# Kernel tuning notes

Measured on AMD Instinct MI355X. Metric: run time of the kernel, lower is better.

## Reference

```python
import jax, jax.numpy as jnp
import numpy as np

L, H, P, R = 8192, 1024, 512, 256


def setup_inputs() -> dict:
    key = jax.random.key(0)
    ks = jax.random.split(key, 12)
    nrm = lambda k, s, std=0.01: std * jax.random.normal(k, s, dtype=jnp.float32)
    # Stable complex diagonal: |Lambda_bar| in [0.8, 0.999)
    mag = 0.8 + 0.199 * jax.random.uniform(ks[8], (P,), dtype=jnp.float32)
    phase = jnp.pi * jax.random.uniform(ks[9], (P,), dtype=jnp.float32)
    return {
        "input_sequence": jax.random.normal(ks[0], (L, H), dtype=jnp.float32),
        "F": nrm(ks[1], (R, H)),
        "H_proj": nrm(ks[2], (R, H)),
        "Delta_p": jnp.eye(R, dtype=jnp.float32),
        "Delta_r": jnp.eye(R, dtype=jnp.float32),
        "E": nrm(ks[3], (P, R)),
        "G": nrm(ks[4], (H, R)),
        "Lambda_bar_re": (mag * jnp.cos(phase)).astype(jnp.float32),
        "Lambda_bar_im": (mag * jnp.sin(phase)).astype(jnp.float32),
        "B_bar_re": nrm(ks[5], (P, H), 0.05),
        "B_bar_im": nrm(ks[6], (P, H), 0.05),
        "C_re": nrm(ks[7], (H, P), 0.05),
        "C_im": nrm(ks[10], (H, P), 0.05),
        "D": nrm(ks[11], (H, H), 0.02),
    }


def _binop(a, b):
    # Diagonal linear SSM associative combine: (lam, bu)
    return (b[0] * a[0], b[0] * a[1] + b[1])


def reference(input_sequence, F, H_proj, Delta_p, Delta_r, E, G,
              Lambda_bar_re, Lambda_bar_im, B_bar_re, B_bar_im,
              C_re, C_im, D):
    # p_k = Delta_p @ (F @ u_k), r_k = Delta_r @ (H_proj @ u_k)  -- vmapped over L via matmul
    p_seq = (input_sequence @ F.T) @ Delta_p.T            # (L, R)
    r_seq = (input_sequence @ H_proj.T) @ Delta_r.T       # (L, R)
    up_seq = jnp.concatenate([input_sequence, p_seq], axis=-1)  # (L, H+R)

    Lam = (Lambda_bar_re + 1j * Lambda_bar_im).astype(jnp.complex64)         # (P,)
    B_bar = (B_bar_re + 1j * B_bar_im).astype(jnp.complex64)                 # (P, H)
    B_ext = jnp.concatenate([B_bar, E.astype(jnp.complex64)], axis=1)        # (P, H+R)

    # Per-step driving term Bu_k = B_ext @ up_k
    Bu = up_seq.astype(jnp.complex64) @ B_ext.T                               # (L, P)
    Lam_el = jnp.broadcast_to(Lam, Bu.shape)                                  # (L, P)

    # Parallel associative scan: x_k = Lam * x_{k-1} + Bu_k
    _, xs = jax.lax.associative_scan(_binop, (Lam_el, Bu))                    # (L, P)

    C_tilde = (C_re + 1j * C_im).astype(jnp.complex64)                        # (H, P)
    # conj_sym=True branch: y_k = 2*Re(C_tilde @ x_k) + G @ r_k + D @ u_k
    y_seq = (2.0 * jnp.real(xs @ C_tilde.T)
             + r_seq @ G.T
             + input_sequence @ D.T)                                           # (L, H)
    return y_seq
```

## Files before the change

### kernel.cpp

```cpp
#include <hip/hip_runtime.h>
#include <stdint.h>

#define L_SEQ 8192
#define NCHUNK 64
#define CHUNK  128

typedef __attribute__((ext_vector_type(8))) short bf16x8;
typedef __attribute__((ext_vector_type(4))) float f32x4;

__device__ inline unsigned short f2bf(float x) {
  unsigned u = __builtin_bit_cast(unsigned, x);
  unsigned r = (u + 0x7fffu + ((u >> 16) & 1u)) >> 16;
  return (unsigned short)r;
}
__device__ inline float bf2f(unsigned short b) {
  unsigned u = ((unsigned)b) << 16;
  return __builtin_bit_cast(float, u);
}

#define GLD16(g, l)                                                            \
  __builtin_amdgcn_global_load_lds(                                            \
      (const __attribute__((address_space(1))) unsigned int*)(g),              \
      (__attribute__((address_space(3))) unsigned int*)(l), 16, 0, 0)

__global__ __launch_bounds__(256) void prep(
    const float* __restrict__ F, const float* __restrict__ Hp,
    const float* __restrict__ dP, const float* __restrict__ dR,
    const float* __restrict__ E, const float* __restrict__ G,
    const float* __restrict__ Bim, const float* __restrict__ Cre,
    const float* __restrict__ Cim, const float* __restrict__ u,
    unsigned short* __restrict__ Ft, unsigned short* __restrict__ Ht,
    unsigned short* __restrict__ dPb, unsigned short* __restrict__ dRb,
    unsigned short* __restrict__ Eb, unsigned short* __restrict__ Gb,
    unsigned short* __restrict__ W1, unsigned short* __restrict__ Wy,
    unsigned short* __restrict__ A2) {
  __shared__ float tile[32][33];
  const int b = blockIdx.x, tid = threadIdx.x;
  if (b < 512) {
    const float* src = (b < 256) ? F : Hp;
    unsigned short* dst = (b < 256) ? Ft : Ht;
    int bb = b & 255;
    int bx = bb & 31, by = bb >> 5;
    int tx = tid & 31, ty = tid >> 5;
#pragma unroll
    for (int dy = 0; dy < 32; dy += 8)
      tile[ty + dy][tx] = src[(size_t)(by * 32 + ty + dy) * 1024 + bx * 32 + tx];
    __syncthreads();
#pragma unroll
    for (int dy = 0; dy < 32; dy += 8)
      dst[(size_t)(bx * 32 + ty + dy) * 256 + by * 32 + tx] = f2bf(tile[tx][ty + dy]);
    return;
  }
  if (b < 1024) {
    const float* src;
    unsigned short* dst;
    int q;
    if (b < 576)      { src = dP; dst = dPb; q = (b - 512) * 256 + tid; }
    else if (b < 640) { src = dR; dst = dRb; q = (b - 576) * 256 + tid; }
    else if (b < 768) { src = E;  dst = Eb;  q = (b - 640) * 256 + tid; }
    else              { src = G;  dst = Gb;  q = (b - 768) * 256 + tid; }
    int e = q * 4;
    float4 v = *(const float4*)(src + e);
    ushort4 o = {f2bf(v.x), f2bf(v.y), f2bf(v.z), f2bf(v.w)};
    *(ushort4*)(dst + e) = o;
    return;
  }
  if (b < 1536) {
    int q = (b - 1024) * 256 + tid;
    int e = q * 4, p = e >> 10, j = e & 1023;
    float4 v = *(const float4*)(Bim + (size_t)p * 1024 + j);
    ushort4 o = {f2bf(v.x), f2bf(v.y), f2bf(v.z), f2bf(v.w)};
    *(ushort4*)(W1 + (size_t)(2 * p + 1) * 1024 + j) = o;
    return;
  }
  if (b < 2560) {
    int q = (b - 1536) * 256 + tid;
    int i = q >> 8, jp = (q & 255) * 2;
    float2 re = *(const float2*)(Cre + (size_t)i * 512 + jp);
    float2 im = *(const float2*)(Cim + (size_t)i * 512 + jp);
    ushort4 o = {f2bf(2.f * re.x), f2bf(-2.f * im.x), f2bf(2.f * re.y), f2bf(-2.f * im.y)};
    *(ushort4*)(Wy + (size_t)i * 2048 + 1024 + 2 * jp) = o;
    return;
  }
  {
    int q = (b - 2560) * 256 + tid;
    int e = q * 4, i = e >> 10, j = e & 1023;
    float4 v = *(const float4*)(u + (size_t)i * 1024 + j);
    ushort4 o = {f2bf(v.x), f2bf(v.y), f2bf(v.z), f2bf(v.w)};
    *(ushort4*)(A2 + (size_t)i * 2048 + j) = o;
  }
}

template <int HAS_ADD, int OUT_F32, int OUT_BF16>
__device__ __forceinline__ void gemm_body(
    const unsigned short* __restrict__ A, int lda,
    const unsigned short* __restrict__ B, int ldb,
    float* __restrict__ C, int ldc,
    unsigned short* __restrict__ Cb, int ldcb,
    const float* __restrict__ Add, int ldadd, int K, int m0, int n0,
    unsigned short* sA, unsigned short* sB) {
  const int tid = threadIdx.x;
  const int lane = tid & 63, wave = tid >> 6;
  const int wm = wave >> 1, wn = wave & 1;
  const int frow = lane & 15, fg = lane >> 4;

  const int srow = lane >> 2;
  const int scol = (lane & 3) * 8;
  const unsigned short* gA0 = A + (size_t)(m0 + wave * 32 + srow) * lda + scol;
  const unsigned short* gA1 = gA0 + (size_t)16 * lda;
  const unsigned short* gB0 = B + (size_t)(n0 + wave * 32 + srow) * ldb + scol;
  const unsigned short* gB1 = gB0 + (size_t)16 * ldb;

  f32x4 acc[4][4] = {};
  const int nt = K >> 5;

  {
    unsigned short* a0 = sA + wave * 1024;
    unsigned short* b0 = sB + wave * 1024;
    GLD16(gA0, a0); GLD16(gA1, a0 + 512);
    GLD16(gB0, b0); GLD16(gB1, b0 + 512);
  }
  __syncthreads();

  for (int t = 0; t < nt; ++t) {
    const int cur = (t & 1) * 4096;
    if (t + 1 < nt) {
      const int nxt = 4096 - cur;
      const int kt = (t + 1) * 32;
      unsigned short* a0 = sA + nxt + wave * 1024;
      unsigned short* b0 = sB + nxt + wave * 1024;
      GLD16(gA0 + kt, a0); GLD16(gA1 + kt, a0 + 512);
      GLD16(gB0 + kt, b0); GLD16(gB1 + kt, b0 + 512);
    }
    const unsigned short* bA = sA + cur;
    const unsigned short* bB = sB + cur;
    bf16x8 fa[4], fb[4];
#pragma unroll
    for (int f = 0; f < 4; ++f) {
      fa[f] = *(const bf16x8*)(bA + (wm * 64 + f * 16 + frow) * 32 + fg * 8);
      fb[f] = *(const bf16x8*)(bB + (wn * 64 + f * 16 + frow) * 32 + fg * 8);
    }
#pragma unroll
    for (int i = 0; i < 4; ++i)
#pragma unroll
      for (int j = 0; j < 4; ++j)
        acc[i][j] = __builtin_amdgcn_mfma_f32_16x16x32_bf16(fa[i], fb[j], acc[i][j], 0, 0, 0);
    __syncthreads();
  }

  const int crow4 = (lane >> 4) * 4, ccol = lane & 15;
#pragma unroll
  for (int i = 0; i < 4; ++i)
#pragma unroll
    for (int j = 0; j < 4; ++j)
#pragma unroll
      for (int q = 0; q < 4; ++q) {
        int r = m0 + wm * 64 + i * 16 + crow4 + q;
        int c = n0 + wn * 64 + j * 16 + ccol;
        float v = acc[i][j][q];
        if (HAS_ADD) v += Add[(size_t)r * ldadd + c];
        if (OUT_F32) C[(size_t)r * ldc + c] = v;
        if (OUT_BF16) Cb[(size_t)r * ldcb + c] = f2bf(v);
      }
}

template <int HAS_ADD, int OUT_F32, int OUT_BF16>
__global__ __launch_bounds__(256) void gemm_bt(
    const unsigned short* __restrict__ A, int lda,
    const unsigned short* __restrict__ B, int ldb,
    float* __restrict__ C, int ldc,
    unsigned short* __restrict__ Cb, int ldcb,
    const float* __restrict__ Add, int ldadd, int K) {
  __shared__ __align__(16) unsigned short sA[2 * 128 * 32];
  __shared__ __align__(16) unsigned short sB[2 * 128 * 32];
  gemm_body<HAS_ADD, OUT_F32, OUT_BF16>(A, lda, B, ldb, C, ldc, Cb, ldcb, Add,
                                        ldadd, K, blockIdx.x * 128,
                                        blockIdx.y * 128, sA, sB);
}

struct GemmP {
  const unsigned short* A; int lda;
  const unsigned short* B; int ldb;
  float* C; int ldc;
  unsigned short* Cb; int ldcb;
  const float* Add; int ldadd;
  int K; int gx;
};

template <int HAS_ADD, int OUT_F32, int OUT_BF16>
__global__ __launch_bounds__(256) void gemm_bt_dual(GemmP p0, GemmP p1) {
  __shared__ __align__(16) unsigned short sA[2 * 128 * 32];
  __shared__ __align__(16) unsigned short sB[2 * 128 * 32];
  GemmP p = blockIdx.z ? p1 : p0;
  if ((int)blockIdx.x >= p.gx) return;
  gemm_body<HAS_ADD, OUT_F32, OUT_BF16>(p.A, p.lda, p.B, p.ldb, p.C, p.ldc,
                                        p.Cb, p.ldcb, p.Add, p.ldadd, p.K,
                                        blockIdx.x * 128, blockIdx.y * 128, sA, sB);
}

__global__ __launch_bounds__(256) void scan_carry(const unsigned short* __restrict__ Bub,
                                                  const float* __restrict__ lre,
                                                  const float* __restrict__ lim,
                                                  float2* __restrict__ carry2) {
  int g = blockIdx.x * 256 + threadIdx.x;
  int p = g & 511, c = g >> 9;
  float ar = lre[p], ai = lim[p];
  float sr = 0.f, si = 0.f;
  const unsigned short* base = Bub + (size_t)c * CHUNK * 1024 + 2 * p;
#pragma unroll 8
  for (int i = 0; i < CHUNK; ++i) {
    unsigned w = *(const unsigned*)(base + (size_t)i * 1024);
    float br = bf2f((unsigned short)(w & 0xffff));
    float bi = bf2f((unsigned short)(w >> 16));
    float nr = ar * sr - ai * si + br;
    float ni = ar * si + ai * sr + bi;
    sr = nr; si = ni;
  }
  carry2[(size_t)p * NCHUNK + c] = make_float2(sr, si);
}

__global__ __launch_bounds__(512) void scan_prefix(const float2* __restrict__ carry2,
                                                   const float* __restrict__ lre,
                                                   const float* __restrict__ lim,
                                                   float2* __restrict__ prefix2) {
  int p = threadIdx.x;
  float ar = lre[p], ai = lim[p];
  float cr = ar, ci = ai;
#pragma unroll
  for (int s = 0; s < 7; ++s) {
    float t = cr * cr - ci * ci;
    ci = 2.f * cr * ci;
    cr = t;
  }
  float sr = 0.f, si = 0.f;
  const float2* cp = carry2 + (size_t)p * NCHUNK;
  float2* pp = prefix2 + (size_t)p * NCHUNK;
  for (int cb = 0; cb < NCHUNK; cb += 16) {
    float2 cv[16];
#pragma unroll
    for (int i = 0; i < 16; ++i) cv[i] = cp[cb + i];
#pragma unroll
    for (int i = 0; i < 16; ++i) {
      float nr = cr * sr - ci * si + cv[i].x;
      float ni = cr * si + ci * sr + cv[i].y;
      sr = nr; si = ni;
      pp[cb + i] = make_float2(sr, si);
    }
  }
}

__global__ __launch_bounds__(256) void scan_apply(const unsigned short* __restrict__ Bub,
                                                  const float* __restrict__ lre,
                                                  const float* __restrict__ lim,
                                                  const float2* __restrict__ prefix2,
                                                  unsigned short* __restrict__ A2) {
  int g = blockIdx.x * 256 + threadIdx.x;
  int p = g & 511, c = g >> 9;
  float ar = lre[p], ai = lim[p];
  float sr = 0.f, si = 0.f;
  if (c > 0) {
    float2 pr = prefix2[(size_t)p * NCHUNK + c - 1];
    sr = pr.x; si = pr.y;
  }
  const unsigned short* base = Bub + (size_t)c * CHUNK * 1024 + 2 * p;
  unsigned* ob = (unsigned*)(A2 + (size_t)c * CHUNK * 2048 + 1024 + 2 * p);
#pragma unroll 8
  for (int i = 0; i < CHUNK; ++i) {
    unsigned w = *(const unsigned*)(base + (size_t)i * 1024);
    float br = bf2f((unsigned short)(w & 0xffff));
    float bi = bf2f((unsigned short)(w >> 16));
    float nr = ar * sr - ai * si + br;
    float ni = ar * si + ai * sr + bi;
    sr = nr; si = ni;
    ob[(size_t)i * 1024] = (unsigned)f2bf(sr) | ((unsigned)f2bf(si) << 16);
  }
}

extern "C" void kernel_launch(void* const* d_in, const int* in_sizes, int n_in,
                              void* d_out, int out_size, void* d_ws, size_t ws_size,
                              hipStream_t stream) {
  const float* u   = (const float*)d_in[0];
  const float* F   = (const float*)d_in[1];
  const float* Hp  = (const float*)d_in[2];
  const float* dP  = (const float*)d_in[3];
  const float* dR  = (const float*)d_in[4];
  const float* E   = (const float*)d_in[5];
  const float* G   = (const float*)d_in[6];
  const float* lre = (const float*)d_in[7];
  const float* lim = (const float*)d_in[8];
  const float* Bre = (const float*)d_in[9];
  const float* Bim = (const float*)d_in[10];
  const float* Cre = (const float*)d_in[11];
  const float* Cim = (const float*)d_in[12];
  const float* Dm  = (const float*)d_in[13];
  float* y = (float*)d_out;

  uint8_t* ws = (uint8_t*)d_ws;
  size_t off = 0;
  auto alloc = [&](size_t bytes) {
    void* p = ws + off;
    off += (bytes + 255) & ~(size_t)255;
    return p;
  };
  unsigned short* A2  = (unsigned short*)alloc((size_t)L_SEQ * 2048 * 2);
  unsigned short* W1  = (unsigned short*)alloc((size_t)1024 * 1024 * 2);
  unsigned short* Wy  = (unsigned short*)alloc((size_t)1024 * 2048 * 2);
  unsigned short* Bub = (unsigned short*)alloc((size_t)L_SEQ * 1024 * 2);
  unsigned short* Ft  = (unsigned short*)alloc((size_t)1024 * 256 * 2);
  unsigned short* Ht  = (unsigned short*)alloc((size_t)1024 * 256 * 2);
  unsigned short* FpT = (unsigned short*)alloc((size_t)1024 * 256 * 2);
  unsigned short* HrT = (unsigned short*)alloc((size_t)1024 * 256 * 2);
  unsigned short* dPb = (unsigned short*)alloc((size_t)256 * 256 * 2);
  unsigned short* dRb = (unsigned short*)alloc((size_t)256 * 256 * 2);
  unsigned short* Eb  = (unsigned short*)alloc((size_t)512 * 256 * 2);
  unsigned short* Gb  = (unsigned short*)alloc((size_t)1024 * 256 * 2);
  float* carry  = (float*)alloc((size_t)512 * NCHUNK * 8);
  float* prefix = (float*)alloc((size_t)512 * NCHUNK * 8);
  (void)ws_size; (void)in_sizes; (void)n_in; (void)out_size;

  prep<<<10752, 256, 0, stream>>>(F, Hp, dP, dR, E, G, Bim, Cre, Cim, u,
                                  Ft, Ht, dPb, dRb, Eb, Gb, W1, Wy, A2);

  GemmP pa = {Ft, 256, dPb, 256, nullptr, 0, FpT, 256, nullptr, 0, 256, 8};
  GemmP pb = {Ht, 256, dRb, 256, nullptr, 0, HrT, 256, nullptr, 0, 256, 8};
  gemm_bt_dual<0, 0, 1><<<dim3(8, 2, 2), 256, 0, stream>>>(pa, pb);

  GemmP pc = {Eb, 256, FpT, 256, nullptr, 0, W1, 2048, Bre, 1024, 256, 4};
  GemmP pd = {Gb, 256, HrT, 256, nullptr, 0, Wy, 2048, Dm, 1024, 256, 8};
  gemm_bt_dual<1, 0, 1><<<dim3(8, 8, 2), 256, 0, stream>>>(pc, pd);

  gemm_bt<0, 0, 1><<<dim3(64, 8), 256, 0, stream>>>(A2, 2048, W1, 1024, nullptr, 0,
                                                    Bub, 1024, nullptr, 0, 1024);

  scan_carry<<<128, 256, 0, stream>>>(Bub, lre, lim, (float2*)carry);
  scan_prefix<<<1, 512, 0, stream>>>((const float2*)carry, lre, lim, (float2*)prefix);
  scan_apply<<<128, 256, 0, stream>>>(Bub, lre, lim, (const float2*)prefix, A2);

  gemm_bt<0, 1, 0><<<dim3(64, 8), 256, 0, stream>>>(A2, 2048, Wy, 2048, y, 1024,
                                                    nullptr, 0, nullptr, 0, 2048);
}
```

Baseline: 241.0 us.

## Triple-buffer GEMM loads, swizzle blocks per XCD, fold small matmuls and scan prefix

The GEMM main loop moves from a double-buffered loop with a full barrier every step to a three-stage LDS pipeline that waits on vmcnt, so global loads stay in flight while MFMAs run. gemm_bt now remaps block indices so neighbouring tiles land on the same XCD, aiming for better L2 reuse. The weight pre-products E@Delta_p and G@Delta_r are computed directly in the prep kernel with a naive fp32 loop, and the reassociation (G·Δr)·H_proj replaces G·(Δr·H_proj), which removes one dual GEMM launch. The single-block scan_prefix kernel is dropped; each scan_apply thread now serially combines the earlier chunk carries itself, which adds redundant work in exchange for one fewer launch.

```diff
diff --git a/kernel.cpp b/kernel.cpp
--- a/kernel.cpp
+++ b/kernel.cpp
@@ -30,8 +30,7 @@
     const float* __restrict__ Bim, const float* __restrict__ Cre,
     const float* __restrict__ Cim, const float* __restrict__ u,
     unsigned short* __restrict__ Ft, unsigned short* __restrict__ Ht,
-    unsigned short* __restrict__ dPb, unsigned short* __restrict__ dRb,
-    unsigned short* __restrict__ Eb, unsigned short* __restrict__ Gb,
+    unsigned short* __restrict__ T1b, unsigned short* __restrict__ T2b,
     unsigned short* __restrict__ W1, unsigned short* __restrict__ Wy,
     unsigned short* __restrict__ A2) {
   __shared__ float tile[32][33];
@@ -52,29 +51,33 @@
     return;
   }
   if (b < 1024) {
-    const float* src;
-    unsigned short* dst;
-    int q;
-    if (b < 576)      { src = dP; dst = dPb; q = (b - 512) * 256 + tid; }
-    else if (b < 640) { src = dR; dst = dRb; q = (b - 576) * 256 + tid; }
-    else if (b < 768) { src = E;  dst = Eb;  q = (b - 640) * 256 + tid; }
-    else              { src = G;  dst = Gb;  q = (b - 768) * 256 + tid; }
-    int e = q * 4;
-    float4 v = *(const float4*)(src + e);
-    ushort4 o = {f2bf(v.x), f2bf(v.y), f2bf(v.z), f2bf(v.w)};
-    *(ushort4*)(dst + e) = o;
-    return;
-  }
-  if (b < 1536) {
-    int q = (b - 1024) * 256 + tid;
+    int i = b - 512, j = tid;
+    const float* Er = E + (size_t)i * 256;
+    float acc = 0.f;
+#pragma unroll 8
+    for (int k = 0; k < 256; ++k) acc += Er[k] * dP[(size_t)k * 256 + j];
+    T1b[(size_t)i * 256 + j] = f2bf(acc);
+    return;
+  }
+  if (b < 2048) {
+    int i = b - 1024, j = tid;
+    const float* Gr = G + (size_t)i * 256;
+    float acc = 0.f;
+#pragma unroll 8
+    for (int k = 0; k < 256; ++k) acc += Gr[k] * dR[(size_t)k * 256 + j];
+    T2b[(size_t)i * 256 + j] = f2bf(acc);
+    return;
+  }
+  if (b < 2560) {
+    int q = (b - 2048) * 256 + tid;
     int e = q * 4, p = e >> 10, j = e & 1023;
     float4 v = *(const float4*)(Bim + (size_t)p * 1024 + j);
     ushort4 o = {f2bf(v.x), f2bf(v.y), f2bf(v.z), f2bf(v.w)};
     *(ushort4*)(W1 + (size_t)(2 * p + 1) * 1024 + j) = o;
     return;
   }
-  if (b < 2560) {
-    int q = (b - 1536) * 256 + tid;
+  if (b < 3584) {
+    int q = (b - 2560) * 256 + tid;
     int i = q >> 8, jp = (q & 255) * 2;
     float2 re = *(const float2*)(Cre + (size_t)i * 512 + jp);
     float2 im = *(const float2*)(Cim + (size_t)i * 512 + jp);
@@ -83,7 +86,7 @@
     return;
   }
   {
-    int q = (b - 2560) * 256 + tid;
+    int q = (b - 3584) * 256 + tid;
     int e = q * 4, i = e >> 10, j = e & 1023;
     float4 v = *(const float4*)(u + (size_t)i * 1024 + j);
     ushort4 o = {f2bf(v.x), f2bf(v.y), f2bf(v.z), f2bf(v.w)};
@@ -114,26 +117,16 @@
   f32x4 acc[4][4] = {};
   const int nt = K >> 5;
 
-  {
-    unsigned short* a0 = sA + wave * 1024;
-    unsigned short* b0 = sB + wave * 1024;
-    GLD16(gA0, a0); GLD16(gA1, a0 + 512);
-    GLD16(gB0, b0); GLD16(gB1, b0 + 512);
-  }
-  __syncthreads();
-
-  for (int t = 0; t < nt; ++t) {
-    const int cur = (t & 1) * 4096;
-    if (t + 1 < nt) {
-      const int nxt = 4096 - cur;
-      const int kt = (t + 1) * 32;
-      unsigned short* a0 = sA + nxt + wave * 1024;
-      unsigned short* b0 = sB + nxt + wave * 1024;
-      GLD16(gA0 + kt, a0); GLD16(gA1 + kt, a0 + 512);
-      GLD16(gB0 + kt, b0); GLD16(gB1 + kt, b0 + 512);
-    }
-    const unsigned short* bA = sA + cur;
-    const unsigned short* bB = sB + cur;
+  auto STAGE = [&](int t, int buf) {
+    const int kt = t * 32;
+    unsigned short* a0 = sA + buf * 4096 + wave * 1024;
+    unsigned short* b0 = sB + buf * 4096 + wave * 1024;
+    GLD16(gA0 + kt, a0); GLD16(gA1 + kt, a0 + 512);
+    GLD16(gB0 + kt, b0); GLD16(gB1 + kt, b0 + 512);
+  };
+  auto COMPUTE = [&](int buf) {
+    const unsigned short* bA = sA + buf * 4096;
+    const unsigned short* bB = sB + buf * 4096;
     bf16x8 fa[4], fb[4];
 #pragma unroll
     for (int f = 0; f < 4; ++f) {
@@ -145,8 +138,27 @@
 #pragma unroll
       for (int j = 0; j < 4; ++j)
         acc[i][j] = __builtin_amdgcn_mfma_f32_16x16x32_bf16(fa[i], fb[j], acc[i][j], 0, 0, 0);
-    __syncthreads();
-  }
+  };
+
+  STAGE(0, 0);
+  if (nt > 1) STAGE(1, 1);
+
+  int buf = 0;
+  for (int t = 0; t < nt - 1; ++t) {
+    asm volatile("s_waitcnt vmcnt(4)" ::: "memory");
+    __builtin_amdgcn_s_barrier();
+    __builtin_amdgcn_sched_barrier(0);
+    if (t + 2 < nt) {
+      int b2 = buf + 2; if (b2 >= 3) b2 -= 3;
+      STAGE(t + 2, b2);
+    }
+    COMPUTE(buf);
+    if (++buf == 3) buf = 0;
+  }
+  asm volatile("s_waitcnt vmcnt(0)" ::: "memory");
+  __builtin_amdgcn_s_barrier();
+  __builtin_amdgcn_sched_barrier(0);
+  COMPUTE(buf);
 
   const int crow4 = (lane >> 4) * 4, ccol = lane & 15;
 #pragma unroll
@@ -171,11 +183,14 @@
     float* __restrict__ C, int ldc,
     unsigned short* __restrict__ Cb, int ldcb,
     const float* __restrict__ Add, int ldadd, int K) {
-  __shared__ __align__(16) unsigned short sA[2 * 128 * 32];
-  __shared__ __align__(16) unsigned short sB[2 * 128 * 32];
+  __shared__ __align__(16) unsigned short sA[3 * 128 * 32];
+  __shared__ __align__(16) unsigned short sB[3 * 128 * 32];
+  int lin = blockIdx.y * gridDim.x + blockIdx.x;
+  int xcd = lin & 7, idx = lin >> 3;
+  int bx = xcd * 8 + (idx & 7);
+  int by = idx >> 3;
   gemm_body<HAS_ADD, OUT_F32, OUT_BF16>(A, lda, B, ldb, C, ldc, Cb, ldcb, Add,
-                                        ldadd, K, blockIdx.x * 128,
-                                        blockIdx.y * 128, sA, sB);
+                                        ldadd, K, bx * 128, by * 128, sA, sB);
 }
 
 struct GemmP {
@@ -189,8 +204,8 @@
 
 template <int HAS_ADD, int OUT_F32, int OUT_BF16>
 __global__ __launch_bounds__(256) void gemm_bt_dual(GemmP p0, GemmP p1) {
-  __shared__ __align__(16) unsigned short sA[2 * 128 * 32];
-  __shared__ __align__(16) unsigned short sB[2 * 128 * 32];
+  __shared__ __align__(16) unsigned short sA[3 * 128 * 32];
+  __shared__ __align__(16) unsigned short sB[3 * 128 * 32];
   GemmP p = blockIdx.z ? p1 : p0;
   if ((int)blockIdx.x >= p.gx) return;
   gemm_body<HAS_ADD, OUT_F32, OUT_BF16>(p.A, p.lda, p.B, p.ldb, p.C, p.ldc,
@@ -216,14 +231,16 @@
     float ni = ar * si + ai * sr + bi;
     sr = nr; si = ni;
   }
-  carry2[(size_t)p * NCHUNK + c] = make_float2(sr, si);
-}
-
-__global__ __launch_bounds__(512) void scan_prefix(const float2* __restrict__ carry2,
-                                                   const float* __restrict__ lre,
-                                                   const float* __restrict__ lim,
-                                                   float2* __restrict__ prefix2) {
-  int p = threadIdx.x;
+  carry2[(size_t)c * 512 + p] = make_float2(sr, si);
+}
+
+__global__ __launch_bounds__(256) void scan_apply(const unsigned short* __restrict__ Bub,
+                                                  const float* __restrict__ lre,
+                                                  const float* __restrict__ lim,
+                                                  const float2* __restrict__ carry2,
+                                                  unsigned short* __restrict__ A2) {
+  int g = blockIdx.x * 256 + threadIdx.x;
+  int p = g & 511, c = g >> 9;
   float ar = lre[p], ai = lim[p];
   float cr = ar, ci = ai;
 #pragma unroll
@@ -233,34 +250,11 @@
     cr = t;
   }
   float sr = 0.f, si = 0.f;
-  const float2* cp = carry2 + (size_t)p * NCHUNK;
-  float2* pp = prefix2 + (size_t)p * NCHUNK;
-  for (int cb = 0; cb < NCHUNK; cb += 16) {
-    float2 cv[16];
-#pragma unroll
-    for (int i = 0; i < 16; ++i) cv[i] = cp[cb + i];
-#pragma unroll
-    for (int i = 0; i < 16; ++i) {
-      float nr = cr * sr - ci * si + cv[i].x;
-      float ni = cr * si + ci * sr + cv[i].y;
-      sr = nr; si = ni;
-      pp[cb + i] = make_float2(sr, si);
-    }
-  }
-}
-
-__global__ __launch_bounds__(256) void scan_apply(const unsigned short* __restrict__ Bub,
-                                                  const float* __restrict__ lre,
-                                                  const float* __restrict__ lim,
-                                                  const float2* __restrict__ prefix2,
-                                                  unsigned short* __restrict__ A2) {
-  int g = blockIdx.x * 256 + threadIdx.x;
-  int p = g & 511, c = g >> 9;
-  float ar = lre[p], ai = lim[p];
-  float sr = 0.f, si = 0.f;
-  if (c > 0) {
-    float2 pr = prefix2[(size_t)p * NCHUNK + c - 1];
-    sr = pr.x; si = pr.y;
+  for (int cc = 0; cc < c; ++cc) {
+    float2 cv = carry2[(size_t)cc * 512 + p];
+    float nr = cr * sr - ci * si + cv.x;
+    float ni = cr * si + ci * sr + cv.y;
+    sr = nr; si = ni;
   }
   const unsigned short* base = Bub + (size_t)c * CHUNK * 1024 + 2 * p;
   unsigned* ob = (unsigned*)(A2 + (size_t)c * CHUNK * 2048 + 1024 + 2 * p);
@@ -308,33 +302,23 @@
   unsigned short* Bub = (unsigned short*)alloc((size_t)L_SEQ * 1024 * 2);
   unsigned short* Ft  = (unsigned short*)alloc((size_t)1024 * 256 * 2);
   unsigned short* Ht  = (unsigned short*)alloc((size_t)1024 * 256 * 2);
-  unsigned short* FpT = (unsigned short*)alloc((size_t)1024 * 256 * 2);
-  unsigned short* HrT = (unsigned short*)alloc((size_t)1024 * 256 * 2);
-  unsigned short* dPb = (unsigned short*)alloc((size_t)256 * 256 * 2);
-  unsigned short* dRb = (unsigned short*)alloc((size_t)256 * 256 * 2);
-  unsigned short* Eb  = (unsigned short*)alloc((size_t)512 * 256 * 2);
-  unsigned short* Gb  = (unsigned short*)alloc((size_t)1024 * 256 * 2);
-  float* carry  = (float*)alloc((size_t)512 * NCHUNK * 8);
-  float* prefix = (float*)alloc((size_t)512 * NCHUNK * 8);
+  unsigned short* T1b = (unsigned short*)alloc((size_t)512 * 256 * 2);
+  unsigned short* T2b = (unsigned short*)alloc((size_t)1024 * 256 * 2);
+  float* carry = (float*)alloc((size_t)NCHUNK * 512 * 8);
   (void)ws_size; (void)in_sizes; (void)n_in; (void)out_size;
 
-  prep<<<10752, 256, 0, stream>>>(F, Hp, dP, dR, E, G, Bim, Cre, Cim, u,
-                                  Ft, Ht, dPb, dRb, Eb, Gb, W1, Wy, A2);
-
-  GemmP pa = {Ft, 256, dPb, 256, nullptr, 0, FpT, 256, nullptr, 0, 256, 8};
-  GemmP pb = {Ht, 256, dRb, 256, nullptr, 0, HrT, 256, nullptr, 0, 256, 8};
-  gemm_bt_dual<0, 0, 1><<<dim3(8, 2, 2), 256, 0, stream>>>(pa, pb);
-
-  GemmP pc = {Eb, 256, FpT, 256, nullptr, 0, W1, 2048, Bre, 1024, 256, 4};
-  GemmP pd = {Gb, 256, HrT, 256, nullptr, 0, Wy, 2048, Dm, 1024, 256, 8};
+  prep<<<11776, 256, 0, stream>>>(F, Hp, dP, dR, E, G, Bim, Cre, Cim, u,
+                                  Ft, Ht, T1b, T2b, W1, Wy, A2);
+
+  GemmP pc = {T1b, 256, Ft, 256, nullptr, 0, W1, 2048, Bre, 1024, 256, 4};
+  GemmP pd = {T2b, 256, Ht, 256, nullptr, 0, Wy, 2048, Dm, 1024, 256, 8};
   gemm_bt_dual<1, 0, 1><<<dim3(8, 8, 2), 256, 0, stream>>>(pc, pd);
 
   gemm_bt<0, 0, 1><<<dim3(64, 8), 256, 0, stream>>>(A2, 2048, W1, 1024, nullptr, 0,
                                                     Bub, 1024, nullptr, 0, 1024);
 
   scan_carry<<<128, 256, 0, stream>>>(Bub, lre, lim, (float2*)carry);
-  scan_prefix<<<1, 512, 0, stream>>>((const float2*)carry, lre, lim, (float2*)prefix);
-  scan_apply<<<128, 256, 0, stream>>>(Bub, lre, lim, (const float2*)prefix, A2);
+  scan_apply<<<128, 256, 0, stream>>>(Bub, lre, lim, (const float2*)carry, A2);
 
   gemm_bt<0, 1, 0><<<dim3(64, 8), 256, 0, stream>>>(A2, 2048, Wy, 2048, y, 1024,
                                                     nullptr, 0, nullptr, 0, 2048);
```

New measurement: 241.4 us. About the same (+0.2%).
